# Kernel tuning notes

Hardware: AMD Instinct MI355X
Metric: run time of the kernel (lower is better)

## Reference

```python
import jax, jax.numpy as jnp
import numpy as np

D_INPUT, D_MODEL, D_STATE, D_DISCR, KER = 1024, 2048, 16, 128, 4

def setup_inputs() -> dict:
    key = jax.random.key(0)
    ks = jax.random.split(key, 10)
    sc = lambda fan_in: 1.0 / np.sqrt(fan_in)
    seq = jax.random.normal(ks[0], (2, 1024, D_INPUT), dtype=jnp.float32)
    W_in = jax.random.uniform(ks[1], (2 * D_MODEL, D_INPUT), jnp.float32, -sc(D_INPUT), sc(D_INPUT))
    W_out = jax.random.uniform(ks[2], (D_INPUT, D_MODEL), jnp.float32, -sc(D_MODEL), sc(D_MODEL))
    W_sB = jax.random.uniform(ks[3], (D_STATE, D_MODEL), jnp.float32, -sc(D_MODEL), sc(D_MODEL))
    W_sC = jax.random.uniform(ks[4], (D_STATE, D_MODEL), jnp.float32, -sc(D_MODEL), sc(D_MODEL))
    W_sD1 = jax.random.uniform(ks[5], (D_DISCR, D_MODEL), jnp.float32, -sc(D_MODEL), sc(D_MODEL))
    W_sD2 = jax.random.uniform(ks[6], (D_MODEL, D_DISCR), jnp.float32, -sc(D_DISCR), sc(D_DISCR))
    conv_w = jax.random.uniform(ks[7], (D_MODEL, 1, KER), jnp.float32, -sc(KER), sc(KER))
    conv_b = jax.random.uniform(ks[8], (D_MODEL,), jnp.float32, -sc(KER), sc(KER))
    A_param = jnp.tile(jnp.arange(1, D_STATE + 1, dtype=jnp.float32), (D_MODEL, 1))
    D_param = jnp.ones((D_MODEL,), dtype=jnp.float32)
    return dict(seq=seq, W_in=W_in, W_out=W_out, W_sB=W_sB, W_sC=W_sC,
                W_sD1=W_sD1, W_sD2=W_sD2, conv_w=conv_w, conv_b=conv_b,
                A_param=A_param, D_param=D_param)

def _mamba_fwd(seq, W_in, W_out, W_sB, W_sC, W_sD1, W_sD2, conv_w, conv_b, A_param, D_param):
    b, l, _ = seq.shape
    ab = seq @ W_in.T                                   # [b,l,2*dm]
    a, g = jnp.split(ab, 2, axis=-1)
    # causal depthwise conv: torch pads ker-1 both sides then trims [..., :l]
    x = jnp.swapaxes(a, 1, 2)                           # [b,dm,l]
    y = jax.lax.conv_general_dilated(
        x, conv_w, window_strides=(1,), padding=[(KER - 1, 0)],
        dimension_numbers=('NCH', 'OIH', 'NCH'), feature_group_count=D_MODEL)
    y = y + conv_b[None, :, None]
    a = jax.nn.silu(jnp.swapaxes(y, 1, 2))              # [b,l,dm]
    # SSM
    B = a @ W_sB.T                                      # [b,l,s]
    C = a @ W_sC.T                                      # [b,l,s]
    s_delta = jax.nn.softplus(D_param + (a @ W_sD1.T) @ W_sD2.T)  # [b,l,dm]
    expA = jnp.exp(-A_param)                            # [dm,s]
    A_bar = expA[None, None] * s_delta[..., None]       # [b,l,dm,s]
    X_bar = B[:, :, None, :] * s_delta[..., None] * a[..., None]  # [b,l,dm,s]
    A_t = jnp.moveaxis(A_bar, 1, 0)                     # [l,b,dm,s]
    X_t = jnp.moveaxis(X_bar, 1, 0)
    h0 = jnp.zeros((b, D_MODEL, D_STATE), dtype=seq.dtype)
    def step(h, ax):
        At, Xt = ax
        h = At * h + Xt
        return h, h
    _, hid = jax.lax.scan(step, h0, (A_t, X_t))         # hid: [l,b,dm,s]
    out_ssm = jnp.einsum('lbds,lbs->lbd', hid, jnp.moveaxis(C, 1, 0))
    out_ssm = jnp.moveaxis(out_ssm, 0, 1) + D_param * a # [b,l,dm]
    out = (out_ssm * jax.nn.silu(g)) @ W_out.T          # [b,l,d_input]
    return out

def reference(seq, W_in, W_out, W_sB, W_sC, W_sD1, W_sD2, conv_w, conv_b, A_param, D_param):
    return _mamba_fwd(seq, W_in, W_out, W_sB, W_sC, W_sD1, W_sD2, conv_w, conv_b, A_param, D_param)
```

## Files before the change

kernel.cpp:

```cpp
#include <hip/hip_runtime.h>
#include <math.h>

#define DI 1024
#define DM 2048
#define DS 16
#define LSEQ 1024
#define NB 2
#define NTOK (NB * LSEQ)
#define TC 128
#define WU 32
#define LDU 164
#define LDP 324

typedef unsigned short ushort_t;
typedef __attribute__((ext_vector_type(8))) short short8;
typedef __attribute__((ext_vector_type(4))) float f32x4;

__device__ __forceinline__ float bf2f(ushort_t u) {
    union { unsigned u; float f; } c; c.u = (unsigned)u << 16; return c.f;
}
__device__ __forceinline__ ushort_t f2bf(float f) {
    union { float f; unsigned u; } c; c.f = f;
    unsigned r = c.u + 0x7FFFu + ((c.u >> 16) & 1u);
    return (ushort_t)(r >> 16);
}

__device__ __forceinline__ void gload16(const void* g, void* l) {
    __builtin_amdgcn_global_load_lds(
        (const __attribute__((address_space(1))) void*)g,
        (__attribute__((address_space(3))) void*)l, 16, 0, 0);
}

template<int CTRL>
__device__ __forceinline__ float dpp_mv(float v) {
    int r = __builtin_amdgcn_update_dpp(0, __builtin_bit_cast(int, v), CTRL, 0xF, 0xF, true);
    return __builtin_bit_cast(float, r);
}
__device__ __forceinline__ float sum8(float v) {
    v += dpp_mv<0xB1>(v);
    v += dpp_mv<0x4E>(v);
    v += dpp_mv<0x141>(v);
    return v;
}

__device__ __forceinline__ void cvt4(const float* __restrict__ in,
                                     ushort_t* __restrict__ out, int q) {
    float4 v = ((const float4*)in)[q];
    ushort4 o;
    o.x = f2bf(v.x); o.y = f2bf(v.y); o.z = f2bf(v.z); o.w = f2bf(v.w);
    ((ushort4*)out)[q] = o;
}

__global__ __launch_bounds__(256) void prep(
    const float* __restrict__ seq, const float* __restrict__ W_in,
    const float* __restrict__ W_out, const float* __restrict__ W_sD2,
    const float* __restrict__ Wb, const float* __restrict__ Wc,
    const float* __restrict__ Wd1,
    ushort_t* __restrict__ seq_bf, ushort_t* __restrict__ W_in_bf,
    ushort_t* __restrict__ W_out_bf, ushort_t* __restrict__ W_sD2_bf,
    ushort_t* __restrict__ wbcd)
{
    int q = blockIdx.x * 256 + threadIdx.x;
    if (q < 524288)        cvt4(seq,   seq_bf,   q);
    else if (q < 1572864)  cvt4(W_in,  W_in_bf,  q - 524288);
    else if (q < 2097152)  cvt4(W_out, W_out_bf, q - 1572864);
    else if (q < 2162688)  cvt4(W_sD2, W_sD2_bf, q - 2097152);
    else {
        int p = q - 2162688;
        int idx = p * 4;
        int row = idx >> 11, col = idx & (DM - 1);
        float4 v = make_float4(0.f, 0.f, 0.f, 0.f);
        if (row < 16)       v = *(const float4*)&Wb[row * DM + col];
        else if (row < 32)  v = *(const float4*)&Wc[(row - 16) * DM + col];
        else if (row < 160) v = *(const float4*)&Wd1[(row - 32) * DM + col];
        ushort4 o;
        o.x = f2bf(v.x); o.y = f2bf(v.y); o.z = f2bf(v.z); o.w = f2bf(v.w);
        ((ushort4*)wbcd)[p] = o;
    }
}

template<int TM, int EPI>
__global__ __launch_bounds__(256) void gemm_bt(
    const ushort_t* __restrict__ A, const ushort_t* __restrict__ B,
    void* __restrict__ Cout, int K, int lda, int ldb, int ldc,
    const float* __restrict__ bias, void* __restrict__ Cpart, size_t pstride)
{
    constexpr int MF = TM / 32;
    __shared__ ushort_t As[TM * 32];
    __shared__ ushort_t Bs[128 * 32];
    const int tid = threadIdx.x;
    const int lane = tid & 63;
    const int wv = tid >> 6;
    const int wr = wv >> 1, wc = wv & 1;

    const int gx = gridDim.x, gy = gridDim.y;
    const int nwg = gx * gy;
    const int orig = blockIdx.y * gx + blockIdx.x;
    const int q8 = nwg >> 3, r8 = nwg & 7;
    const int xcd = orig & 7, i8 = orig >> 3;
    const int wg = ((xcd < r8) ? xcd * (q8 + 1) : r8 * (q8 + 1) + (xcd - r8) * q8) + i8;
    const int bm = (wg / gx) * TM, bn = (wg % gx) * 128;

    int kbeg = 0, kend = K;
    if (EPI == 5) { int ks = K / gridDim.z; kbeg = blockIdx.z * ks; kend = kbeg + ks; }

    f32x4 acc[MF][4];
#pragma unroll
    for (int m = 0; m < MF; ++m)
#pragma unroll
        for (int n = 0; n < 4; ++n) acc[m][n] = (f32x4){0.f, 0.f, 0.f, 0.f};

    const int r_lo = lane >> 2;
    const int s_l = lane & 3;
    const int row0 = wv * 16 + r_lo;
    const int row1 = 64 + wv * 16 + r_lo;
    const int sg0 = s_l ^ ((row0 >> 1) & 3);
    const int sg1 = s_l ^ ((row1 >> 1) & 3);
    const ushort_t* gA0 = A + (size_t)(bm + row0) * lda + sg0 * 8;
    const ushort_t* gA1 = A + (size_t)(bm + row1) * lda + sg1 * 8;
    const ushort_t* gB0 = B + (size_t)(bn + row0) * ldb + sg0 * 8;
    const ushort_t* gB1 = B + (size_t)(bn + row1) * ldb + sg1 * 8;
    ushort_t* lA0 = &As[(wv * 16) * 32];
    ushort_t* lA1 = &As[((TM == 128 ? 64 : 0) + wv * 16) * 32];
    ushort_t* lB0 = &Bs[(wv * 16) * 32];
    ushort_t* lB1 = &Bs[(64 + wv * 16) * 32];

    for (int k = kbeg; k < kend; k += 32) {
        gload16(gA0 + k, lA0);
        if (TM == 128) gload16(gA1 + k, lA1);
        gload16(gB0 + k, lB0);
        gload16(gB1 + k, lB1);
        __syncthreads();
        short8 af[MF], bfr[4];
#pragma unroll
        for (int m = 0; m < MF; ++m) {
            int row = wr * (TM / 2) + m * 16 + (lane & 15);
            int sl = (lane >> 4) ^ ((row >> 1) & 3);
            af[m] = *(const short8*)&As[row * 32 + sl * 8];
        }
#pragma unroll
        for (int n = 0; n < 4; ++n) {
            int row = wc * 64 + n * 16 + (lane & 15);
            int sl = (lane >> 4) ^ ((row >> 1) & 3);
            bfr[n] = *(const short8*)&Bs[row * 32 + sl * 8];
        }
#pragma unroll
        for (int m = 0; m < MF; ++m)
#pragma unroll
            for (int n = 0; n < 4; ++n)
                acc[m][n] = __builtin_amdgcn_mfma_f32_16x16x32_bf16(af[m], bfr[n], acc[m][n], 0, 0, 0);
        __syncthreads();
    }

    const int orow = bm + wr * (TM / 2) + ((lane >> 4) << 2);
    const int ocol = bn + wc * 64 + (lane & 15);
#pragma unroll
    for (int m = 0; m < MF; ++m)
#pragma unroll
        for (int n = 0; n < 4; ++n) {
            int col = ocol + n * 16;
#pragma unroll
            for (int r = 0; r < 4; ++r) {
                int row = orow + m * 16 + r;
                float v = acc[m][n][r];
                if (EPI == 3) {
                    v += bias[col];
                    v = (v > 20.f) ? v : log1pf(__expf(v));
                    ((ushort_t*)Cout)[(size_t)row * ldc + col] = f2bf(v);
                } else if (EPI == 1) {
                    ((ushort_t*)Cout)[(size_t)row * ldc + col] = f2bf(v);
                } else if (EPI == 5) {
                    ((ushort_t*)Cpart + (size_t)blockIdx.z * pstride)[(size_t)row * ldc + col] = f2bf(v);
                } else {
                    ((float*)Cout)[(size_t)row * ldc + col] = v;
                }
            }
        }
}

__global__ __launch_bounds__(256) void reduce_bcd(const ushort_t* __restrict__ part,
                                                  ushort_t* __restrict__ outh)
{
    int q = blockIdx.x * 256 + threadIdx.x;
    float sx = 0.f, sy = 0.f, sz = 0.f, sw = 0.f;
#pragma unroll
    for (int z = 0; z < 8; ++z) {
        ushort4 v = ((const ushort4*)part)[q + z * 131072];
        sx += bf2f(v.x); sy += bf2f(v.y); sz += bf2f(v.z); sw += bf2f(v.w);
    }
    ushort4 o;
    o.x = f2bf(sx); o.y = f2bf(sy); o.z = f2bf(sz); o.w = f2bf(sw);
    ((ushort4*)outh)[q] = o;
}

__global__ __launch_bounds__(256) void reduce_out(const ushort_t* __restrict__ part,
                                                  float* __restrict__ out)
{
    int q = blockIdx.x * 256 + threadIdx.x;
    float sx = 0.f, sy = 0.f, sz = 0.f, sw = 0.f;
#pragma unroll
    for (int z = 0; z < 4; ++z) {
        ushort4 v = ((const ushort4*)part)[q + z * 524288];
        sx += bf2f(v.x); sy += bf2f(v.y); sz += bf2f(v.z); sw += bf2f(v.w);
    }
    float4 o; o.x = sx; o.y = sy; o.z = sz; o.w = sw;
    ((float4*)out)[q] = o;
}

__global__ __launch_bounds__(256) void conv_silu(const ushort_t* __restrict__ ab,
                                                 const float* __restrict__ w,
                                                 const float* __restrict__ bias,
                                                 ushort_t* __restrict__ outh) {
    const int bt = blockIdx.x;
    const int b = bt >> 10, t = bt & (LSEQ - 1);
    const int d = threadIdx.x * 8;

    float wv[8][4];
#pragma unroll
    for (int j = 0; j < 8; ++j) {
        float4 tw = *(const float4*)&w[(d + j) * 4];
        wv[j][0] = tw.x; wv[j][1] = tw.y; wv[j][2] = tw.z; wv[j][3] = tw.w;
    }
    float accv[8];
    {
        float4 b0 = *(const float4*)&bias[d];
        float4 b1 = *(const float4*)&bias[d + 4];
        accv[0] = b0.x; accv[1] = b0.y; accv[2] = b0.z; accv[3] = b0.w;
        accv[4] = b1.x; accv[5] = b1.y; accv[6] = b1.z; accv[7] = b1.w;
    }
#pragma unroll
    for (int k = 0; k < 4; ++k) {
        int tt = t + k - 3;
        if (tt >= 0) {
            short8 av = *(const short8*)&ab[(size_t)(b * LSEQ + tt) * (2 * DM) + d];
#pragma unroll
            for (int j = 0; j < 8; ++j)
                accv[j] = fmaf(bf2f((ushort_t)av[j]), wv[j][k], accv[j]);
        }
    }
    short8 o;
#pragma unroll
    for (int j = 0; j < 8; ++j) {
        float s = accv[j] / (1.f + __expf(-accv[j]));
        o[j] = (short)f2bf(s);
    }
    *(short8*)&outh[(size_t)bt * DM + d] = o;
}

__global__ __launch_bounds__(256) void scan_win(
    const ushort_t* __restrict__ sdel, const ushort_t* __restrict__ aconv,
    const ushort_t* __restrict__ bcd1, const ushort_t* __restrict__ ab,
    const float* __restrict__ A_param, const float* __restrict__ D_param,
    ushort_t* __restrict__ z)
{
    __shared__ ushort_t Ssh[32 * LDU];
    __shared__ ushort_t Vsh[32 * LDU];
    __shared__ float    Bsh[8 * LDP];
    __shared__ float    Csh[8 * LDP];
    __shared__ ushort_t Zsh[TC * 32];

    const int tid = threadIdx.x;
    const int d0 = blockIdx.x * 32;
    const int c = blockIdx.y, b = blockIdx.z;
    const int nw = (c == 0) ? 0 : WU;
    const int nrows = nw + TC;
    const int tok0 = b * LSEQ + c * TC - nw;
    const int tokout0 = b * LSEQ + c * TC;

    for (int j = tid; j < nrows * 8; j += 256) {
        int row = j >> 3, cq = (j & 7) * 4;
        ushort4 sv = *(const ushort4*)&sdel[(size_t)(tok0 + row) * DM + d0 + cq];
        ushort4 vv = *(const ushort4*)&aconv[(size_t)(tok0 + row) * DM + d0 + cq];
        Ssh[(cq + 0) * LDU + row] = sv.x; Ssh[(cq + 1) * LDU + row] = sv.y;
        Ssh[(cq + 2) * LDU + row] = sv.z; Ssh[(cq + 3) * LDU + row] = sv.w;
        Vsh[(cq + 0) * LDU + row] = vv.x; Vsh[(cq + 1) * LDU + row] = vv.y;
        Vsh[(cq + 2) * LDU + row] = vv.z; Vsh[(cq + 3) * LDU + row] = vv.w;
    }
    for (int j = tid; j < nrows * 8; j += 256) {
        int row = j >> 3, p = j & 7;
        int sq = (p & 3) * 4;
        const ushort_t* src = bcd1 + (size_t)(tok0 + row) * 256 + ((p < 4) ? sq : 16 + sq);
        ushort4 v = *(const ushort4*)src;
        float* dst = (p < 4) ? &Bsh[(sq >> 1) * LDP + 2 * row] : &Csh[(sq >> 1) * LDP + 2 * row];
        dst[0] = bf2f(v.x); dst[1] = bf2f(v.y);
        dst[LDP + 0] = bf2f(v.z); dst[LDP + 1] = bf2f(v.w);
    }
    __syncthreads();

    const int q = tid & 7, dl = tid >> 3;
    const int d = d0 + dl;
    float ea0 = __expf(-A_param[d * DS + 2 * q]);
    float ea1 = __expf(-A_param[d * DS + 2 * q + 1]);
    const float Dp = D_param[d];
    float h0 = 0.f, h1 = 0.f;

    for (int i4 = 0; i4 < nw; i4 += 4) {
        ushort4 sdv = *(const ushort4*)&Ssh[dl * LDU + i4];
        ushort4 avv = *(const ushort4*)&Vsh[dl * LDU + i4];
        float4 Bp0 = *(const float4*)&Bsh[q * LDP + 2 * i4];
        float4 Bp1 = *(const float4*)&Bsh[q * LDP + 2 * i4 + 4];
        float sdu[4] = {bf2f(sdv.x), bf2f(sdv.y), bf2f(sdv.z), bf2f(sdv.w)};
        float avu[4] = {bf2f(avv.x), bf2f(avv.y), bf2f(avv.z), bf2f(avv.w)};
        float b0u[4] = {Bp0.x, Bp0.z, Bp1.x, Bp1.z};
        float b1u[4] = {Bp0.y, Bp0.w, Bp1.y, Bp1.w};
#pragma unroll
        for (int u = 0; u < 4; ++u) {
            float x = sdu[u] * avu[u];
            h0 = fmaf(sdu[u] * ea0, h0, x * b0u[u]);
            h1 = fmaf(sdu[u] * ea1, h1, x * b1u[u]);
        }
    }
    for (int i4 = nw; i4 < nrows; i4 += 4) {
        ushort4 sdv = *(const ushort4*)&Ssh[dl * LDU + i4];
        ushort4 avv = *(const ushort4*)&Vsh[dl * LDU + i4];
        float4 Bp0 = *(const float4*)&Bsh[q * LDP + 2 * i4];
        float4 Bp1 = *(const float4*)&Bsh[q * LDP + 2 * i4 + 4];
        float4 Cp0 = *(const float4*)&Csh[q * LDP + 2 * i4];
        float4 Cp1 = *(const float4*)&Csh[q * LDP + 2 * i4 + 4];
        float sdu[4] = {bf2f(sdv.x), bf2f(sdv.y), bf2f(sdv.z), bf2f(sdv.w)};
        float avu[4] = {bf2f(avv.x), bf2f(avv.y), bf2f(avv.z), bf2f(avv.w)};
        float b0u[4] = {Bp0.x, Bp0.z, Bp1.x, Bp1.z};
        float b1u[4] = {Bp0.y, Bp0.w, Bp1.y, Bp1.w};
        float c0u[4] = {Cp0.x, Cp0.z, Cp1.x, Cp1.z};
        float c1u[4] = {Cp0.y, Cp0.w, Cp1.y, Cp1.w};
        float rv0, rv1, rv2, rv3;
        {
            float x, r;
            x = sdu[0] * avu[0];
            h0 = fmaf(sdu[0] * ea0, h0, x * b0u[0]); h1 = fmaf(sdu[0] * ea1, h1, x * b1u[0]);
            r = sum8(fmaf(h1, c1u[0], h0 * c0u[0])); rv0 = fmaf(Dp, avu[0], r);
            x = sdu[1] * avu[1];
            h0 = fmaf(sdu[1] * ea0, h0, x * b0u[1]); h1 = fmaf(sdu[1] * ea1, h1, x * b1u[1]);
            r = sum8(fmaf(h1, c1u[1], h0 * c0u[1])); rv1 = fmaf(Dp, avu[1], r);
            x = sdu[2] * avu[2];
            h0 = fmaf(sdu[2] * ea0, h0, x * b0u[2]); h1 = fmaf(sdu[2] * ea1, h1, x * b1u[2]);
            r = sum8(fmaf(h1, c1u[2], h0 * c0u[2])); rv2 = fmaf(Dp, avu[2], r);
            x = sdu[3] * avu[3];
            h0 = fmaf(sdu[3] * ea0, h0, x * b0u[3]); h1 = fmaf(sdu[3] * ea1, h1, x * b1u[3]);
            r = sum8(fmaf(h1, c1u[3], h0 * c0u[3])); rv3 = fmaf(Dp, avu[3], r);
        }
        float rvq = (q == 0) ? rv0 : (q == 1) ? rv1 : (q == 2) ? rv2 : rv3;
        int io = i4 - nw;
        if (q < 4) Zsh[(io + q) * 32 + dl] = f2bf(rvq);
    }
    __syncthreads();
    for (int j = tid; j < TC * 8; j += 256) {
        int row = j >> 3, cq = (j & 7) * 4;
        ushort4 ov = *(const ushort4*)&Zsh[row * 32 + cq];
        ushort4 gv = *(const ushort4*)&ab[(size_t)(tokout0 + row) * (2 * DM) + DM + d0 + cq];
        ushort4 o;
        float g0 = bf2f(gv.x), g1 = bf2f(gv.y), g2 = bf2f(gv.z), g3 = bf2f(gv.w);
        o.x = f2bf(bf2f(ov.x) * (g0 / (1.f + __expf(-g0))));
        o.y = f2bf(bf2f(ov.y) * (g1 / (1.f + __expf(-g1))));
        o.z = f2bf(bf2f(ov.z) * (g2 / (1.f + __expf(-g2))));
        o.w = f2bf(bf2f(ov.w) * (g3 / (1.f + __expf(-g3))));
        *(ushort4*)&z[(size_t)(tokout0 + row) * DM + d0 + cq] = o;
    }
}

extern "C" void kernel_launch(void* const* d_in, const int* in_sizes, int n_in,
                              void* d_out, int out_size, void* d_ws, size_t ws_size,
                              hipStream_t stream) {
    const float* seq    = (const float*)d_in[0];
    const float* W_in   = (const float*)d_in[1];
    const float* W_out  = (const float*)d_in[2];
    const float* W_sB   = (const float*)d_in[3];
    const float* W_sC   = (const float*)d_in[4];
    const float* W_sD1  = (const float*)d_in[5];
    const float* W_sD2  = (const float*)d_in[6];
    const float* conv_w = (const float*)d_in[7];
    const float* conv_b = (const float*)d_in[8];
    const float* A_par  = (const float*)d_in[9];
    const float* D_par  = (const float*)d_in[10];
    float* out = (float*)d_out;

    char* ws = (char*)d_ws;
    const size_t MiB = 1024 * 1024;
    ushort_t* ab_bf    = (ushort_t*)(ws);
    ushort_t* part_out = (ushort_t*)(ws);
    ushort_t* aconv_h  = (ushort_t*)(ws + 16 * MiB);
    ushort_t* sdel_h   = (ushort_t*)(ws + 24 * MiB);
    ushort_t* W_out_bf = (ushort_t*)(ws + 32 * MiB);
    ushort_t* bcd1     = (ushort_t*)(ws + 36 * MiB);
    ushort_t* W_sD2_bf = (ushort_t*)(ws + 37 * MiB);
    ushort_t* Wbcd     = (ushort_t*)(ws + 37 * MiB + 512*1024);
    ushort_t* seq_bf   = (ushort_t*)(ws + 39 * MiB);
    ushort_t* W_in_bf  = (ushort_t*)(ws + 43 * MiB);
    ushort_t* partK    = (ushort_t*)(ws + 43 * MiB);
    ushort_t* z_bf     = (ushort_t*)(ws + 63 * MiB);

    dim3 blk(256);

    prep<<<dim3(8960), blk, 0, stream>>>(seq, W_in, W_out, W_sD2, W_sB, W_sC, W_sD1,
                                         seq_bf, W_in_bf, W_out_bf, W_sD2_bf, Wbcd);

    gemm_bt<64, 1><<<dim3(32, 32), blk, 0, stream>>>(seq_bf, W_in_bf, ab_bf, 1024, DI, DI, 2 * DM, nullptr, nullptr, 0);

    conv_silu<<<dim3(NTOK), blk, 0, stream>>>(ab_bf, conv_w, conv_b, aconv_h);

    gemm_bt<64, 5><<<dim3(2, 32, 8), blk, 0, stream>>>(aconv_h, Wbcd, nullptr, DM, DM, DM, 256, nullptr, partK, 2048 * 256);

    reduce_bcd<<<dim3(512), blk, 0, stream>>>(partK, bcd1);

    gemm_bt<64, 3><<<dim3(16, 32), blk, 0, stream>>>(bcd1 + 32, W_sD2_bf, sdel_h, 128, 256, 128, DM, D_par, nullptr, 0);

    scan_win<<<dim3(DM / 32, LSEQ / TC, NB), blk, 0, stream>>>(
        sdel_h, aconv_h, bcd1, ab_bf, A_par, D_par, z_bf);

    gemm_bt<64, 5><<<dim3(8, 32, 4), blk, 0, stream>>>(z_bf, W_out_bf, nullptr, DM, DM, DM, DI, nullptr, part_out, 2048 * 1024);

    reduce_out<<<dim3(2048), blk, 0, stream>>>(part_out, out);
}
```

Baseline: 145.8 us.

## Double-buffer LDS tiles in bf16 GEMM to overlap loads with MFMA

The GEMM main loop now keeps two LDS buffers for the A and B tiles. It prefetches the next K-slice with direct global-to-LDS loads while the current slice feeds the MFMAs, which removes one of the two barriers per iteration. The goal is to hide global load latency behind compute. The cost is twice the LDS use, which may lower occupancy. Correctness depends on gload16 completing before the single barrier at the end of each iteration.

```diff
diff --git a/kernel.cpp b/kernel.cpp
--- a/kernel.cpp
+++ b/kernel.cpp
@@ -86,8 +86,10 @@
     const float* __restrict__ bias, void* __restrict__ Cpart, size_t pstride)
 {
     constexpr int MF = TM / 32;
-    __shared__ ushort_t As[TM * 32];
-    __shared__ ushort_t Bs[128 * 32];
+    constexpr int ASZ = TM * 32;
+    constexpr int BSZ = 128 * 32;
+    __shared__ ushort_t As[2 * ASZ];
+    __shared__ ushort_t Bs[2 * BSZ];
     const int tid = threadIdx.x;
     const int lane = tid & 63;
     const int wv = tid >> 6;
@@ -120,29 +122,39 @@
     const ushort_t* gA1 = A + (size_t)(bm + row1) * lda + sg1 * 8;
     const ushort_t* gB0 = B + (size_t)(bn + row0) * ldb + sg0 * 8;
     const ushort_t* gB1 = B + (size_t)(bn + row1) * ldb + sg1 * 8;
-    ushort_t* lA0 = &As[(wv * 16) * 32];
-    ushort_t* lA1 = &As[((TM == 128 ? 64 : 0) + wv * 16) * 32];
-    ushort_t* lB0 = &Bs[(wv * 16) * 32];
-    ushort_t* lB1 = &Bs[(64 + wv * 16) * 32];
-
+    const int lA0o = (wv * 16) * 32;
+    const int lA1o = ((TM == 128 ? 64 : 0) + wv * 16) * 32;
+    const int lB0o = (wv * 16) * 32;
+    const int lB1o = (64 + wv * 16) * 32;
+
+    gload16(gA0 + kbeg, &As[lA0o]);
+    if (TM == 128) gload16(gA1 + kbeg, &As[lA1o]);
+    gload16(gB0 + kbeg, &Bs[lB0o]);
+    gload16(gB1 + kbeg, &Bs[lB1o]);
+    __syncthreads();
+
+    int cur = 0;
     for (int k = kbeg; k < kend; k += 32) {
-        gload16(gA0 + k, lA0);
-        if (TM == 128) gload16(gA1 + k, lA1);
-        gload16(gB0 + k, lB0);
-        gload16(gB1 + k, lB1);
-        __syncthreads();
+        const int nxt = cur ^ 1;
+        if (k + 32 < kend) {
+            gload16(gA0 + k + 32, &As[nxt * ASZ + lA0o]);
+            if (TM == 128) gload16(gA1 + k + 32, &As[nxt * ASZ + lA1o]);
+            gload16(gB0 + k + 32, &Bs[nxt * BSZ + lB0o]);
+            gload16(gB1 + k + 32, &Bs[nxt * BSZ + lB1o]);
+        }
+        const int ca = cur * ASZ, cb = cur * BSZ;
         short8 af[MF], bfr[4];
 #pragma unroll
         for (int m = 0; m < MF; ++m) {
             int row = wr * (TM / 2) + m * 16 + (lane & 15);
             int sl = (lane >> 4) ^ ((row >> 1) & 3);
-            af[m] = *(const short8*)&As[row * 32 + sl * 8];
+            af[m] = *(const short8*)&As[ca + row * 32 + sl * 8];
         }
 #pragma unroll
         for (int n = 0; n < 4; ++n) {
             int row = wc * 64 + n * 16 + (lane & 15);
             int sl = (lane >> 4) ^ ((row >> 1) & 3);
-            bfr[n] = *(const short8*)&Bs[row * 32 + sl * 8];
+            bfr[n] = *(const short8*)&Bs[cb + row * 32 + sl * 8];
         }
 #pragma unroll
         for (int m = 0; m < MF; ++m)
@@ -150,6 +162,7 @@
             for (int n = 0; n < 4; ++n)
                 acc[m][n] = __builtin_amdgcn_mfma_f32_16x16x32_bf16(af[m], bfr[n], acc[m][n], 0, 0, 0);
         __syncthreads();
+        cur = nxt;
     }
 
     const int orow = bm + wr * (TM / 2) + ((lane >> 4) << 2);
```

Result: no change. 144.8 us (-0.6%).
